# Optimization experiments

Hardware: AMD Instinct MI355X
Metric: run time of the kernel (lower is better)

## Reference

```python
import jax, jax.numpy as jnp
import numpy as np

N_CLASSES = 256
PER_CLASS = 128
N_SUPPORT = 5
N_QUERY = PER_CLASS - N_SUPPORT  # 123
N_VIEW = 2
D = 384
N = N_CLASSES * PER_CLASS  # 32768


def setup_inputs() -> dict:
    key = jax.random.key(0)
    k1, k2 = jax.random.split(key, 2)
    reps = jax.random.normal(k1, (N, N_VIEW, D), dtype=jnp.float32)
    # block-sorted labels: class c occupies rows [c*PER_CLASS, (c+1)*PER_CLASS)
    labels = (jnp.arange(N, dtype=jnp.int32) // PER_CLASS).astype(jnp.int32)
    return {"reps": reps, "labels": labels}


def reference(reps, labels):
    # labels are block-sorted per class, so the original's
    # labels.eq(c).nonzero()[:n_support] / [n_support:] gathers are static reshapes.
    reps_r = reps.reshape(N_CLASSES, PER_CLASS, N_VIEW, D)
    # class-mean prototypes over the support set: [C, V, D]
    prototypes = reps_r[:, :N_SUPPORT].mean(axis=1)
    # query samples: [C*N_QUERY, V, D]
    queries = reps_r[:, N_SUPPORT:].reshape(N_CLASSES * N_QUERY, N_VIEW, D)

    x2 = jnp.sum(queries * queries, axis=-1)            # [n, V]
    y2 = jnp.sum(prototypes * prototypes, axis=-1)      # [m, V]
    xy = jnp.einsum('nvd,mvd->nmv', queries, prototypes)  # [n, m, V]
    dists = x2[:, None, :] + y2[None, :, :] - 2.0 * xy

    # log_softmax over the prototype (class) axis
    log_p_y = jax.nn.log_softmax(-dists, axis=1)
    log_p_y = log_p_y.reshape(N_CLASSES, N_QUERY, N_CLASSES, N_VIEW)

    # gather the true-class log-prob for each query / view
    cls = jnp.arange(N_CLASSES)
    correct = log_p_y[cls, :, cls, :]  # [C, N_QUERY, V]
    loss = -correct.mean()
    return loss
```

## Files before the change

kernel.cpp:

```cpp
#include <hip/hip_runtime.h>
#include <hip/hip_bf16.h>
#include <math.h>

#define NCLS 256
#define PER_CLASS 128
#define NSUP 5
#define NQRY 123
#define NVIEW 2
#define DD 384
#define NQ_TOT (NCLS * NQRY)
#define BM 128
#define BK 32
#define NKT (DD / BK)
#define QS 40

typedef __attribute__((ext_vector_type(8))) short short8;
typedef __attribute__((ext_vector_type(4))) float floatx4;

union FragU { uint4 u; short8 s; };
union PkU { __hip_bfloat162 b2; unsigned int u; };

__device__ __forceinline__ unsigned int cvt2bf(float lo, float hi) {
    PkU p;
    p.b2 = __float22bfloat162_rn(make_float2(lo, hi));
    return p.u;
}

#define BARRIER() asm volatile("s_waitcnt lgkmcnt(0)\n\ts_barrier" ::: "memory")

__global__ __launch_bounds__(384) void proto_kernel(const float* __restrict__ reps,
                                                    ushort* __restrict__ pbf,
                                                    float* __restrict__ y2) {
    __shared__ float wp[6];
    const int b = blockIdx.x;
    const int c = b & 255, v = b >> 8;
    const int d = threadIdx.x;
    const float* p = reps + ((size_t)(c * PER_CLASS) * NVIEW + v) * DD + d;
    float s = 0.f;
#pragma unroll
    for (int k = 0; k < NSUP; ++k) s += p[(size_t)k * NVIEW * DD];
    s *= 0.2f;
    __hip_bfloat16 h = __float2bfloat16(s);
    pbf[(size_t)b * DD + d] = *reinterpret_cast<ushort*>(&h);
    float q = s * s;
#pragma unroll
    for (int o = 1; o < 64; o <<= 1) q += __shfl_xor(q, o);
    if ((d & 63) == 0) wp[d >> 6] = q;
    __syncthreads();
    if (d == 0) y2[b] = wp[0] + wp[1] + wp[2] + wp[3] + wp[4] + wp[5];
}

__global__ __launch_bounds__(256, 2) void main_kernel(const float* __restrict__ reps,
                                                      const ushort* __restrict__ pbf,
                                                      const float* __restrict__ y2g,
                                                      float* __restrict__ out) {
    __shared__ ushort q_lds[2][BM * QS];
    __shared__ ushort p_lds[2][NCLS * QS];
    __shared__ float pmx[BM][2];
    __shared__ float pse[BM][2];
    __shared__ float wred[8];

    const int t = threadIdx.x;
    const int v = blockIdx.y;
    const int q0 = blockIdx.x * BM;
    const int wave = t >> 6;
    const int lane = t & 63;
    const int col = lane & 15;
    const int quad = lane >> 4;
    const int wm = wave >> 1;
    const int wn = wave & 1;

    const int sq = t >> 1;
    const int h16 = (t & 1) * 16;
    const int nq = q0 + sq;
    const float* qsrc = reps +
        (size_t)((nq / NQRY) * PER_CLASS + NSUP + (nq % NQRY)) * (NVIEW * DD) + v * DD + h16;
    const ushort* psrc = pbf + (size_t)(v * NCLS + t) * DD;

    floatx4 acc[4][8];
#pragma unroll
    for (int mt = 0; mt < 4; ++mt)
#pragma unroll
        for (int nt = 0; nt < 8; ++nt) acc[mt][nt] = (floatx4)0.f;

    float4 qf[4];
    uint4 pl[4];

#define LOADT(kt)                                                                  \
    do {                                                                           \
        _Pragma("unroll") for (int i = 0; i < 4; ++i)                              \
            qf[i] = *(const float4*)(qsrc + (kt) * BK + i * 4);                    \
        _Pragma("unroll") for (int i = 0; i < 4; ++i)                              \
            pl[i] = *((const uint4*)(psrc + (kt) * BK) + i);                       \
    } while (0)

#define STAGE(b)                                                                   \
    do {                                                                           \
        uint4 qw0, qw1;                                                            \
        qw0.x = cvt2bf(qf[0].x, qf[0].y); qw0.y = cvt2bf(qf[0].z, qf[0].w);        \
        qw0.z = cvt2bf(qf[1].x, qf[1].y); qw0.w = cvt2bf(qf[1].z, qf[1].w);        \
        qw1.x = cvt2bf(qf[2].x, qf[2].y); qw1.y = cvt2bf(qf[2].z, qf[2].w);        \
        qw1.z = cvt2bf(qf[3].x, qf[3].y); qw1.w = cvt2bf(qf[3].z, qf[3].w);        \
        *(uint4*)&q_lds[b][sq * QS + h16] = qw0;                                   \
        *(uint4*)&q_lds[b][sq * QS + h16 + 8] = qw1;                               \
        _Pragma("unroll") for (int i = 0; i < 4; ++i)                              \
            *(uint4*)&p_lds[b][t * QS + i * 8] = pl[i];                            \
    } while (0)

#define COMPUTE(b)                                                                 \
    do {                                                                           \
        short8 af[4];                                                              \
        _Pragma("unroll") for (int mt = 0; mt < 4; ++mt) {                         \
            FragU f;                                                               \
            f.u = *(const uint4*)&q_lds[b][(wm * 64 + mt * 16 + col) * QS + quad * 8]; \
            af[mt] = f.s;                                                          \
        }                                                                          \
        _Pragma("unroll") for (int nt = 0; nt < 8; ++nt) {                         \
            FragU bb;                                                              \
            bb.u = *(const uint4*)&p_lds[b][(wn * 128 + nt * 16 + col) * QS + quad * 8]; \
            _Pragma("unroll") for (int mt = 0; mt < 4; ++mt)                       \
                acc[mt][nt] = __builtin_amdgcn_mfma_f32_16x16x32_bf16(af[mt], bb.s, acc[mt][nt], 0, 0, 0); \
        }                                                                          \
    } while (0)

    LOADT(0);
    STAGE(0);
    LOADT(1);
    BARRIER();
#pragma unroll
    for (int kt = 0; kt < NKT; ++kt) {
        COMPUTE(kt & 1);
        if (kt < NKT - 1) {
            STAGE((kt + 1) & 1);
            if (kt < NKT - 2) LOADT(kt + 2);
            BARRIER();
        }
    }

    float y2c[8];
#pragma unroll
    for (int nt = 0; nt < 8; ++nt) y2c[nt] = y2g[v * NCLS + wn * 128 + nt * 16 + col];

    float corr = 0.f;
#pragma unroll
    for (int mt = 0; mt < 4; ++mt) {
#pragma unroll
        for (int r = 0; r < 4; ++r) {
            const int qloc = wm * 64 + mt * 16 + quad * 4 + r;
            const int n = q0 + qloc;
            const int cn = n / NQRY;
            float s[8];
            float mx = -1e30f;
#pragma unroll
            for (int nt = 0; nt < 8; ++nt) {
                s[nt] = 2.f * acc[mt][nt][r] - y2c[nt];
                mx = fmaxf(mx, s[nt]);
                if (cn == wn * 128 + nt * 16 + col) corr += s[nt];
            }
#pragma unroll
            for (int o = 1; o < 16; o <<= 1) mx = fmaxf(mx, __shfl_xor(mx, o));
            float e = 0.f;
#pragma unroll
            for (int nt = 0; nt < 8; ++nt) e += __expf(s[nt] - mx);
#pragma unroll
            for (int o = 1; o < 16; o <<= 1) e += __shfl_xor(e, o);
            if (col == 0) { pmx[qloc][wn] = mx; pse[qloc][wn] = e; }
        }
    }
#pragma unroll
    for (int o = 1; o < 64; o <<= 1) corr += __shfl_xor(corr, o);
    if (lane == 0) wred[wave] = corr;
    __syncthreads();

    float lval = 0.f;
    if (t < BM) {
        float m0 = pmx[t][0], m1 = pmx[t][1];
        float M = fmaxf(m0, m1);
        float E = pse[t][0] * __expf(m0 - M) + pse[t][1] * __expf(m1 - M);
        lval = M + __logf(E);
    }
#pragma unroll
    for (int o = 1; o < 64; o <<= 1) lval += __shfl_xor(lval, o);
    if (lane == 0) wred[4 + wave] = lval;
    __syncthreads();

    if (t == 0) {
        float tot = (wred[4] + wred[5] + wred[6] + wred[7]) -
                    (wred[0] + wred[1] + wred[2] + wred[3]);
        atomicAdd(out, tot * (1.f / (float)(NQ_TOT * NVIEW)));
    }
}

extern "C" void kernel_launch(void* const* d_in, const int* in_sizes, int n_in,
                              void* d_out, int out_size, void* d_ws, size_t ws_size,
                              hipStream_t stream) {
    const float* reps = (const float*)d_in[0];
    float* ws = (float*)d_ws;
    ushort* pbf = (ushort*)ws;
    float* y2 = (float*)(pbf + NVIEW * NCLS * DD);
    float* out = (float*)d_out;

    hipMemsetAsync(out, 0, sizeof(float), stream);
    proto_kernel<<<dim3(NVIEW * NCLS), dim3(DD), 0, stream>>>(reps, pbf, y2);
    main_kernel<<<dim3(NQ_TOT / BM, NVIEW), dim3(256), 0, stream>>>(reps, pbf, y2, out);
}
```

Measured before the change: 166.0 us.

## Halve query tile and load A fragments directly from global into registers

Shrinks the query tile per block from 128 to 64 rows. The query operand is no longer staged through LDS: each lane loads its MFMA A-fragment straight from global memory, converts it to bf16 in registers and prefetches one k-step ahead. Only the prototype tile is double-buffered in LDS, which cuts LDS use and accumulator registers so occupancy can rise to 3 blocks per CU. The trade-off is that each block reuses the prototypes over fewer queries, the block count doubles, and the global query loads are less coalesced. The final reduction is simplified because only t<64 (wave 0) contributes to lval.

```diff
diff --git a/kernel.cpp b/kernel.cpp
--- a/kernel.cpp
+++ b/kernel.cpp
@@ -9,10 +9,10 @@
 #define NVIEW 2
 #define DD 384
 #define NQ_TOT (NCLS * NQRY)
-#define BM 128
+#define BM 64
 #define BK 32
 #define NKT (DD / BK)
-#define QS 40
+#define PSTR 40
 
 typedef __attribute__((ext_vector_type(8))) short short8;
 typedef __attribute__((ext_vector_type(4))) float floatx4;
@@ -50,15 +50,14 @@
     if (d == 0) y2[b] = wp[0] + wp[1] + wp[2] + wp[3] + wp[4] + wp[5];
 }
 
-__global__ __launch_bounds__(256, 2) void main_kernel(const float* __restrict__ reps,
+__global__ __launch_bounds__(256, 3) void main_kernel(const float* __restrict__ reps,
                                                       const ushort* __restrict__ pbf,
                                                       const float* __restrict__ y2g,
                                                       float* __restrict__ out) {
-    __shared__ ushort q_lds[2][BM * QS];
-    __shared__ ushort p_lds[2][NCLS * QS];
+    __shared__ ushort p_lds[2][NCLS * PSTR];
     __shared__ float pmx[BM][2];
     __shared__ float pse[BM][2];
-    __shared__ float wred[8];
+    __shared__ float cred[4];
 
     const int t = threadIdx.x;
     const int v = blockIdx.y;
@@ -70,69 +69,68 @@
     const int wm = wave >> 1;
     const int wn = wave & 1;
 
-    const int sq = t >> 1;
-    const int h16 = (t & 1) * 16;
-    const int nq = q0 + sq;
-    const float* qsrc = reps +
-        (size_t)((nq / NQRY) * PER_CLASS + NSUP + (nq % NQRY)) * (NVIEW * DD) + v * DD + h16;
+    const int r0 = q0 + wm * 32 + col;
+    const int r1 = r0 + 16;
+    const float* a0 = reps +
+        (size_t)((r0 / NQRY) * PER_CLASS + NSUP + (r0 % NQRY)) * (NVIEW * DD) + v * DD + quad * 8;
+    const float* a1 = reps +
+        (size_t)((r1 / NQRY) * PER_CLASS + NSUP + (r1 % NQRY)) * (NVIEW * DD) + v * DD + quad * 8;
     const ushort* psrc = pbf + (size_t)(v * NCLS + t) * DD;
 
-    floatx4 acc[4][8];
-#pragma unroll
-    for (int mt = 0; mt < 4; ++mt)
-#pragma unroll
-        for (int nt = 0; nt < 8; ++nt) acc[mt][nt] = (floatx4)0.f;
+    floatx4 acc[2][8];
+#pragma unroll
+    for (int m = 0; m < 2; ++m)
+#pragma unroll
+        for (int nt = 0; nt < 8; ++nt) acc[m][nt] = (floatx4)0.f;
 
     float4 qf[4];
     uint4 pl[4];
 
-#define LOADT(kt)                                                                  \
-    do {                                                                           \
-        _Pragma("unroll") for (int i = 0; i < 4; ++i)                              \
-            qf[i] = *(const float4*)(qsrc + (kt) * BK + i * 4);                    \
-        _Pragma("unroll") for (int i = 0; i < 4; ++i)                              \
-            pl[i] = *((const uint4*)(psrc + (kt) * BK) + i);                       \
+#define ALOAD(kt)                                                          \
+    do {                                                                   \
+        qf[0] = *(const float4*)(a0 + (kt) * BK);                          \
+        qf[1] = *(const float4*)(a0 + (kt) * BK + 4);                      \
+        qf[2] = *(const float4*)(a1 + (kt) * BK);                          \
+        qf[3] = *(const float4*)(a1 + (kt) * BK + 4);                      \
     } while (0)
 
-#define STAGE(b)                                                                   \
-    do {                                                                           \
-        uint4 qw0, qw1;                                                            \
-        qw0.x = cvt2bf(qf[0].x, qf[0].y); qw0.y = cvt2bf(qf[0].z, qf[0].w);        \
-        qw0.z = cvt2bf(qf[1].x, qf[1].y); qw0.w = cvt2bf(qf[1].z, qf[1].w);        \
-        qw1.x = cvt2bf(qf[2].x, qf[2].y); qw1.y = cvt2bf(qf[2].z, qf[2].w);        \
-        qw1.z = cvt2bf(qf[3].x, qf[3].y); qw1.w = cvt2bf(qf[3].z, qf[3].w);        \
-        *(uint4*)&q_lds[b][sq * QS + h16] = qw0;                                   \
-        *(uint4*)&q_lds[b][sq * QS + h16 + 8] = qw1;                               \
-        _Pragma("unroll") for (int i = 0; i < 4; ++i)                              \
-            *(uint4*)&p_lds[b][t * QS + i * 8] = pl[i];                            \
+#define PLOAD(kt)                                                          \
+    do {                                                                   \
+        _Pragma("unroll") for (int i = 0; i < 4; ++i)                      \
+            pl[i] = *((const uint4*)(psrc + (kt) * BK) + i);               \
     } while (0)
 
-#define COMPUTE(b)                                                                 \
-    do {                                                                           \
-        short8 af[4];                                                              \
-        _Pragma("unroll") for (int mt = 0; mt < 4; ++mt) {                         \
-            FragU f;                                                               \
-            f.u = *(const uint4*)&q_lds[b][(wm * 64 + mt * 16 + col) * QS + quad * 8]; \
-            af[mt] = f.s;                                                          \
-        }                                                                          \
-        _Pragma("unroll") for (int nt = 0; nt < 8; ++nt) {                         \
-            FragU bb;                                                              \
-            bb.u = *(const uint4*)&p_lds[b][(wn * 128 + nt * 16 + col) * QS + quad * 8]; \
-            _Pragma("unroll") for (int mt = 0; mt < 4; ++mt)                       \
-                acc[mt][nt] = __builtin_amdgcn_mfma_f32_16x16x32_bf16(af[mt], bb.s, acc[mt][nt], 0, 0, 0); \
-        }                                                                          \
+#define PSTAGE(b)                                                          \
+    do {                                                                   \
+        _Pragma("unroll") for (int i = 0; i < 4; ++i)                      \
+            *(uint4*)&p_lds[b][t * PSTR + i * 8] = pl[i];                  \
     } while (0)
 
-    LOADT(0);
-    STAGE(0);
-    LOADT(1);
+    ALOAD(0);
+    PLOAD(0);
+    PSTAGE(0);
+    PLOAD(1);
     BARRIER();
+
 #pragma unroll
     for (int kt = 0; kt < NKT; ++kt) {
-        COMPUTE(kt & 1);
+        FragU A0, A1;
+        A0.u.x = cvt2bf(qf[0].x, qf[0].y); A0.u.y = cvt2bf(qf[0].z, qf[0].w);
+        A0.u.z = cvt2bf(qf[1].x, qf[1].y); A0.u.w = cvt2bf(qf[1].z, qf[1].w);
+        A1.u.x = cvt2bf(qf[2].x, qf[2].y); A1.u.y = cvt2bf(qf[2].z, qf[2].w);
+        A1.u.z = cvt2bf(qf[3].x, qf[3].y); A1.u.w = cvt2bf(qf[3].z, qf[3].w);
+        if (kt < NKT - 1) ALOAD(kt + 1);
+
+#pragma unroll
+        for (int nt = 0; nt < 8; ++nt) {
+            FragU B;
+            B.u = *(const uint4*)&p_lds[kt & 1][(wn * 128 + nt * 16 + col) * PSTR + quad * 8];
+            acc[0][nt] = __builtin_amdgcn_mfma_f32_16x16x32_bf16(A0.s, B.s, acc[0][nt], 0, 0, 0);
+            acc[1][nt] = __builtin_amdgcn_mfma_f32_16x16x32_bf16(A1.s, B.s, acc[1][nt], 0, 0, 0);
+        }
         if (kt < NKT - 1) {
-            STAGE((kt + 1) & 1);
-            if (kt < NKT - 2) LOADT(kt + 2);
+            PSTAGE((kt + 1) & 1);
+            if (kt < NKT - 2) PLOAD(kt + 2);
             BARRIER();
         }
     }
@@ -143,10 +141,10 @@
 
     float corr = 0.f;
 #pragma unroll
-    for (int mt = 0; mt < 4; ++mt) {
+    for (int mt = 0; mt < 2; ++mt) {
 #pragma unroll
         for (int r = 0; r < 4; ++r) {
-            const int qloc = wm * 64 + mt * 16 + quad * 4 + r;
+            const int qloc = wm * 32 + mt * 16 + quad * 4 + r;
             const int n = q0 + qloc;
             const int cn = n / NQRY;
             float s[8];
@@ -169,7 +167,7 @@
     }
 #pragma unroll
     for (int o = 1; o < 64; o <<= 1) corr += __shfl_xor(corr, o);
-    if (lane == 0) wred[wave] = corr;
+    if (lane == 0) cred[wave] = corr;
     __syncthreads();
 
     float lval = 0.f;
@@ -181,12 +179,8 @@
     }
 #pragma unroll
     for (int o = 1; o < 64; o <<= 1) lval += __shfl_xor(lval, o);
-    if (lane == 0) wred[4 + wave] = lval;
-    __syncthreads();
-
     if (t == 0) {
-        float tot = (wred[4] + wred[5] + wred[6] + wred[7]) -
-                    (wred[0] + wred[1] + wred[2] + wred[3]);
+        float tot = lval - (cred[0] + cred[1] + cred[2] + cred[3]);
         atomicAdd(out, tot * (1.f / (float)(NQ_TOT * NVIEW)));
     }
 }
```

Measured after the change: 203.1 us. 22.4% more time.
